# Optimization experiments

Measured on AMD Instinct MI355X. Metric: run time of the kernel, lower is better.

The kernel has to match this reference:

```python
import math
import jax, jax.numpy as jnp
import numpy as np

B, T, C, H = 2, 2048, 1024, 16
D = C // H


def get_slopes(n):
    def pow2_slopes(n):
        start = 2.0 ** (-(2.0 ** (-(math.log2(n) - 3))))
        return [start * (start ** i) for i in range(n)]
    if math.log2(n).is_integer():
        return pow2_slopes(n)
    c = 2 ** math.floor(math.log2(n))
    return pow2_slopes(c) + get_slopes(2 * c)[0::2][: n - c]


def setup_inputs() -> dict:
    key = jax.random.key(0)
    ks = jax.random.split(key, 5)
    std = 0.02
    x = jax.random.normal(ks[0], (B, T, C), dtype=jnp.float32)
    Wq = std * jax.random.normal(ks[1], (C, C), dtype=jnp.float32)
    Wk = std * jax.random.normal(ks[2], (C, C), dtype=jnp.float32)
    Wv = std * jax.random.normal(ks[3], (C, C), dtype=jnp.float32)
    Wo = (std / math.sqrt(24)) * jax.random.normal(ks[4], (C, C), dtype=jnp.float32)
    z = jnp.zeros((C,), dtype=jnp.float32)
    return {"x": x, "Wq": Wq, "bq": z, "Wk": Wk, "bk": z, "Wv": Wv, "bv": z, "Wo": Wo, "bo": z}


def reference(x, Wq, bq, Wk, bk, Wv, bv, Wo, bo):
    b, t, c = x.shape
    h, d = H, c // H
    # qkv projections: nn.Linear computes x @ W.T + b
    q = (x @ Wq.T + bq).reshape(b, t, h, d).transpose(0, 2, 1, 3)  # [B,H,T,D]
    k = (x @ Wk.T + bk).reshape(b, t, h, d).transpose(0, 2, 1, 3)
    v = (x @ Wv.T + bv).reshape(b, t, h, d).transpose(0, 2, 1, 3)

    att = jnp.einsum("bhqd,bhkd->bhqk", q, k) * (1.0 / math.sqrt(d))

    # ALiBi bias: -slope_h * (i - j) on the lower triangle, 0 above
    slopes = jnp.asarray(get_slopes(h), dtype=x.dtype)  # [H]
    i = jnp.arange(t)
    rel = jnp.tril(i[:, None] - i[None, :]).astype(x.dtype)  # [T,T]
    alibi = -slopes[:, None, None] * rel  # [H,T,T]
    att = att + alibi[None, :, :, :]

    causal = jnp.tril(jnp.ones((t, t), dtype=bool))
    att = jnp.where(causal[None, None, :, :], att, -jnp.inf)
    att = jax.nn.softmax(att, axis=-1)

    y = jnp.einsum("bhqk,bhkd->bhqd", att, v)
    y = y.transpose(0, 2, 1, 3).reshape(b, t, c)
    return y @ Wo.T + bo
```

## Files before the change

### kernel.cpp

```cpp
#include <hip/hip_runtime.h>
#include <hip/hip_bf16.h>
#include <cstdint>
#include <cstddef>

#define B_ 2
#define T_ 2048
#define C_ 1024
#define H_ 16
#define D_ 64
#define BT_ (B_*T_)
#define QKV_S 3072

typedef __bf16 bf16;
typedef __bf16 bf16x4 __attribute__((ext_vector_type(4)));
typedef __bf16 bf16x8 __attribute__((ext_vector_type(8)));
typedef float f32x4 __attribute__((ext_vector_type(4)));

__global__ __launch_bounds__(256) void cast_f32_bf16(const float* __restrict__ in,
                                                     bf16* __restrict__ out, int n) {
  int stride = gridDim.x * blockDim.x;
  for (int i = blockIdx.x * blockDim.x + threadIdx.x; i * 4 < n; i += stride) {
    float4 v = *reinterpret_cast<const float4*>(in + (size_t)i * 4);
    bf16x4 o;
    o[0] = (bf16)v.x; o[1] = (bf16)v.y; o[2] = (bf16)v.z; o[3] = (bf16)v.w;
    *reinterpret_cast<bf16x4*>(out + (size_t)i * 4) = o;
  }
}

template<typename OutT>
__global__ __launch_bounds__(256) void gemm_bt(const bf16* __restrict__ A,
                                               const bf16* __restrict__ Bm,
                                               const float* __restrict__ bias,
                                               OutT* __restrict__ Cout,
                                               int M, int N, int K) {
  __shared__ bf16 As[128 * 32];
  __shared__ bf16 Bs[128 * 32];
  const int tid = threadIdx.x;
  const int wid = tid >> 6, lane = tid & 63;
  const int grp = lane >> 4, li = lane & 15;
  const int wr = wid >> 1, wc = wid & 1;
  const int m0 = blockIdx.y * 128, n0 = blockIdx.x * 128;

  f32x4 acc[4][4] = {};

  const int srow = lane >> 2;
  const int scol = (lane & 3) * 8;

  for (int k0 = 0; k0 < K; k0 += 32) {
#pragma unroll
    for (int p = 0; p < 2; ++p) {
      const int rbase = (p * 4 + wid) * 16;
      const bf16* ga = A + (size_t)(m0 + rbase + srow) * K + (k0 + scol);
      const bf16* gb = Bm + (size_t)(n0 + rbase + srow) * K + (k0 + scol);
      bf16* la = As + (p * 4 + wid) * 512;
      bf16* lb = Bs + (p * 4 + wid) * 512;
      __builtin_amdgcn_global_load_lds((__attribute__((address_space(1))) void*)ga,
                                       (__attribute__((address_space(3))) void*)la, 16, 0, 0);
      __builtin_amdgcn_global_load_lds((__attribute__((address_space(1))) void*)gb,
                                       (__attribute__((address_space(3))) void*)lb, 16, 0, 0);
    }
    __syncthreads();

    bf16x8 af[4], bfr[4];
#pragma unroll
    for (int m = 0; m < 4; ++m)
      af[m] = *reinterpret_cast<const bf16x8*>(&As[(wr * 64 + m * 16 + li) * 32 + grp * 8]);
#pragma unroll
    for (int n = 0; n < 4; ++n)
      bfr[n] = *reinterpret_cast<const bf16x8*>(&Bs[(wc * 64 + n * 16 + li) * 32 + grp * 8]);
#pragma unroll
    for (int m = 0; m < 4; ++m)
#pragma unroll
      for (int n = 0; n < 4; ++n)
        acc[m][n] = __builtin_amdgcn_mfma_f32_16x16x32_bf16(af[m], bfr[n], acc[m][n], 0, 0, 0);
    __syncthreads();
  }

  float bcol[4];
#pragma unroll
  for (int n = 0; n < 4; ++n) bcol[n] = bias[n0 + wc * 64 + n * 16 + li];
#pragma unroll
  for (int m = 0; m < 4; ++m) {
#pragma unroll
    for (int n = 0; n < 4; ++n) {
      const int col = n0 + wc * 64 + n * 16 + li;
#pragma unroll
      for (int j = 0; j < 4; ++j) {
        const int row = m0 + wr * 64 + m * 16 + grp * 4 + j;
        float v = acc[m][n][j] + bcol[n];
        Cout[(size_t)row * N + col] = (OutT)v;
      }
    }
  }
}

__global__ __launch_bounds__(256) void transpose_v(const bf16* __restrict__ qkv,
                                                   bf16* __restrict__ Vt) {
  __shared__ bf16 tile[64 * 72];
  const int tid = threadIdx.x;
  const int t0 = blockIdx.x * 64, bh = blockIdx.y;
  const int b = bh >> 4, h = bh & 15;
#pragma unroll
  for (int p = 0; p < 2; ++p) {
    int idx = p * 256 + tid;
    int r = idx >> 3, c = (idx & 7) * 8;
    bf16x8 v = *reinterpret_cast<const bf16x8*>(qkv + (size_t)(b * T_ + t0 + r) * QKV_S + 2 * C_ + h * D_ + c);
    *reinterpret_cast<bf16x8*>(&tile[r * 72 + c]) = v;
  }
  __syncthreads();
#pragma unroll
  for (int p = 0; p < 2; ++p) {
    int idx = p * 256 + tid;
    int d = idx >> 3, tc = (idx & 7) * 8;
    bf16x8 o;
#pragma unroll
    for (int j = 0; j < 8; ++j) o[j] = tile[(tc + j) * 72 + d];
    *reinterpret_cast<bf16x8*>(Vt + ((size_t)bh * D_ + d) * T_ + t0 + tc) = o;
  }
}

__global__ __launch_bounds__(512) void attn_kernel(const bf16* __restrict__ qkv,
                                                   const bf16* __restrict__ Vt,
                                                   bf16* __restrict__ Y) {
  __shared__ bf16 Ks[2][64 * 64];
  __shared__ bf16 Vs[2][64 * 64];
  __shared__ bf16 Ps[8 * 16 * 72];

  const int tid = threadIdx.x;
  const int wid = tid >> 6, lane = tid & 63;
  const int grp = lane >> 4, li = lane & 15;
  const int QT = gridDim.x - 1 - blockIdx.x;
  const int bh = blockIdx.y;
  const int b = bh >> 4, h = bh & 15;
  const int q0 = QT * 128;
  const int wq0 = q0 + wid * 16;
  const int qi = wq0 + li;
  const float slope = exp2f(-0.5f * (float)(h + 1));

  bf16* Pw = Ps + wid * (16 * 72);

  bf16x8 qf[2];
  {
    const bf16* qrow = qkv + (size_t)(b * T_ + qi) * QKV_S + h * D_;
    qf[0] = *reinterpret_cast<const bf16x8*>(qrow + grp * 8);
    qf[1] = *reinterpret_cast<const bf16x8*>(qrow + 32 + grp * 8);
#pragma unroll
    for (int c = 0; c < 2; ++c)
#pragma unroll
      for (int j = 0; j < 8; ++j)
        qf[c][j] = (bf16)((float)qf[c][j] * 0.125f);
  }

  f32x4 oacc[4] = {};
  float mrun = -1e30f, lrun = 0.f;

  const bf16* Kbase = qkv + (size_t)b * T_ * QKV_S + C_ + (size_t)h * D_;
  const bf16* Vbase = Vt + (size_t)bh * D_ * T_;

  const int strow = tid >> 3;
  const int stswz = ((tid & 7) * 16) ^ ((strow & 7) << 4);
  const int rsw = (li & 7) << 4;

  auto stage = [&](int kv0, int bufi) __attribute__((always_inline)) {
    const bf16* gk = Kbase + (size_t)(kv0 + strow) * QKV_S + (stswz >> 1);
    const bf16* gv = Vbase + (size_t)strow * T_ + kv0 + (stswz >> 1);
    __builtin_amdgcn_global_load_lds((__attribute__((address_space(1))) void*)gk,
                                     (__attribute__((address_space(3))) void*)(&Ks[bufi][wid * 512]), 16, 0, 0);
    __builtin_amdgcn_global_load_lds((__attribute__((address_space(1))) void*)gv,
                                     (__attribute__((address_space(3))) void*)(&Vs[bufi][wid * 512]), 16, 0, 0);
  };

  auto compute = [&](int kv0, int bufi, bool masked) __attribute__((always_inline)) {
    const char* Kb = (const char*)&Ks[bufi][0];
    const char* Vb = (const char*)&Vs[bufi][0];

    f32x4 s[4] = {};
    __builtin_amdgcn_s_setprio(1);
#pragma unroll
    for (int n = 0; n < 4; ++n) {
      const char* kr = Kb + (n * 16 + li) * 128;
      bf16x8 kf0 = *reinterpret_cast<const bf16x8*>(kr + ((grp * 16) ^ rsw));
      bf16x8 kf1 = *reinterpret_cast<const bf16x8*>(kr + ((64 + grp * 16) ^ rsw));
      s[n] = __builtin_amdgcn_mfma_f32_16x16x32_bf16(kf0, qf[0], s[n], 0, 0, 0);
      s[n] = __builtin_amdgcn_mfma_f32_16x16x32_bf16(kf1, qf[1], s[n], 0, 0, 0);
    }
    __builtin_amdgcn_s_setprio(0);

    float p[4][4];
    float rm = -1e30f;
#pragma unroll
    for (int n = 0; n < 4; ++n)
#pragma unroll
      for (int j = 0; j < 4; ++j) {
        const int kv = kv0 + n * 16 + grp * 4 + j;
        float sv = fmaf(-slope, (float)(qi - kv), s[n][j]);
        if (masked) sv = (kv <= qi) ? sv : -1e30f;
        p[n][j] = sv;
        rm = fmaxf(rm, sv);
      }
    rm = fmaxf(rm, __shfl_xor(rm, 16, 64));
    rm = fmaxf(rm, __shfl_xor(rm, 32, 64));
    const float mnew = fmaxf(mrun, rm);
    const float alpha = __expf(mrun - mnew);
    mrun = mnew;
    float rs = 0.f;
#pragma unroll
    for (int n = 0; n < 4; ++n)
#pragma unroll
      for (int j = 0; j < 4; ++j) {
        float e = __expf(p[n][j] - mnew);
        p[n][j] = e;
        rs += e;
      }
    rs += __shfl_xor(rs, 16, 64);
    rs += __shfl_xor(rs, 32, 64);
    lrun = lrun * alpha + rs;
#pragma unroll
    for (int nd = 0; nd < 4; ++nd)
#pragma unroll
      for (int j = 0; j < 4; ++j)
        oacc[nd][j] *= alpha;

#pragma unroll
    for (int n = 0; n < 4; ++n) {
      bf16x4 p4;
#pragma unroll
      for (int j = 0; j < 4; ++j) p4[j] = (bf16)p[n][j];
      *reinterpret_cast<bf16x4*>(Pw + li * 72 + n * 16 + grp * 4) = p4;
    }
    asm volatile("s_waitcnt lgkmcnt(0)" ::: "memory");
    __builtin_amdgcn_sched_barrier(0);

    __builtin_amdgcn_s_setprio(1);
#pragma unroll
    for (int kc = 0; kc < 2; ++kc) {
      bf16x8 pb = *reinterpret_cast<const bf16x8*>(Pw + li * 72 + kc * 32 + grp * 8);
#pragma unroll
      for (int nd = 0; nd < 4; ++nd) {
        const char* vrp = Vb + (nd * 16 + li) * 128;
        bf16x8 vf = *reinterpret_cast<const bf16x8*>(vrp + ((kc * 64 + grp * 16) ^ rsw));
        oacc[nd] = __builtin_amdgcn_mfma_f32_16x16x32_bf16(vf, pb, oacc[nd], 0, 0, 0);
      }
    }
    __builtin_amdgcn_s_setprio(0);
  };

  const int nt = 2 * QT + 2;
  stage(0, 0);
  __syncthreads();
  int cur = 0;
  for (int t = 0; t < nt; ++t) {
    const int kv0 = t * 64;
    if (t + 1 < nt) stage((t + 1) * 64, cur ^ 1);
    if (kv0 <= wq0) compute(kv0, cur, kv0 + 64 > wq0);
    __syncthreads();
    cur ^= 1;
  }

  const float rinv = 1.f / lrun;
#pragma unroll
  for (int nd = 0; nd < 4; ++nd) {
    bf16x4 o4;
#pragma unroll
    for (int j = 0; j < 4; ++j) o4[j] = (bf16)(oacc[nd][j] * rinv);
    *reinterpret_cast<bf16x4*>(Pw + li * 72 + nd * 16 + grp * 4) = o4;
  }
  asm volatile("s_waitcnt lgkmcnt(0)" ::: "memory");
  __builtin_amdgcn_sched_barrier(0);
  {
    bf16* yrow = Y + (size_t)(b * T_ + qi) * C_ + h * D_;
#pragma unroll
    for (int c = 0; c < 2; ++c) {
      bf16x8 y8 = *reinterpret_cast<const bf16x8*>(Pw + li * 72 + (c * 4 + grp) * 8);
      *reinterpret_cast<bf16x8*>(yrow + (c * 4 + grp) * 8) = y8;
    }
  }
}

extern "C" void kernel_launch(void* const* d_in, const int* in_sizes, int n_in,
                              void* d_out, int out_size, void* d_ws, size_t ws_size,
                              hipStream_t stream) {
  const float* x  = (const float*)d_in[0];
  const float* Wq = (const float*)d_in[1];
  const float* bq = (const float*)d_in[2];
  const float* Wk = (const float*)d_in[3];
  const float* bk = (const float*)d_in[4];
  const float* Wv = (const float*)d_in[5];
  const float* bv = (const float*)d_in[6];
  const float* Wo = (const float*)d_in[7];
  const float* bo = (const float*)d_in[8];
  float* out = (float*)d_out;

  char* ws = (char*)d_ws;
  bf16* xb    = (bf16*)ws; ws += (size_t)BT_ * C_ * 2;
  bf16* wqkvb = (bf16*)ws; ws += (size_t)3 * C_ * C_ * 2;
  bf16* wob   = (bf16*)ws; ws += (size_t)C_ * C_ * 2;
  bf16* qkvb  = (bf16*)ws; ws += (size_t)BT_ * QKV_S * 2;
  bf16* vtb   = (bf16*)ws; ws += (size_t)B_ * H_ * D_ * T_ * 2;
  float* bqkv = (float*)ws; ws += (size_t)3 * C_ * 4;
  bf16* yb    = xb;

  hipMemcpyAsync(bqkv,          bq, C_ * 4, hipMemcpyDeviceToDevice, stream);
  hipMemcpyAsync(bqkv + C_,     bk, C_ * 4, hipMemcpyDeviceToDevice, stream);
  hipMemcpyAsync(bqkv + 2 * C_, bv, C_ * 4, hipMemcpyDeviceToDevice, stream);

  auto cast = [&](const float* src, bf16* dst, int n) {
    int thr = n / 4;
    int blocks = (thr + 255) / 256;
    if (blocks > 4096) blocks = 4096;
    cast_f32_bf16<<<dim3(blocks), dim3(256), 0, stream>>>(src, dst, n);
  };
  cast(x,  xb,  BT_ * C_);
  cast(Wq, wqkvb,               C_ * C_);
  cast(Wk, wqkvb + C_ * C_,     C_ * C_);
  cast(Wv, wqkvb + 2 * C_ * C_, C_ * C_);
  cast(Wo, wob, C_ * C_);

  gemm_bt<bf16><<<dim3(QKV_S / 128, BT_ / 128), dim3(256), 0, stream>>>(xb, wqkvb, bqkv, qkvb, BT_, QKV_S, C_);

  transpose_v<<<dim3(T_ / 64, B_ * H_), dim3(256), 0, stream>>>(qkvb, vtb);

  attn_kernel<<<dim3(T_ / 128, B_ * H_), dim3(512), 0, stream>>>(qkvb, vtb, yb);

  gemm_bt<float><<<dim3(C_ / 128, BT_ / 128), dim3(256), 0, stream>>>(yb, wob, bo, out, BT_, C_, C_);
}
```

Baseline: 243.2 us.

## Fuse casts, double-buffer GEMM, fuse V transpose into QKV GEMM, use exp2 softmax

Merges the five cast launches into one kernel and double-buffers the GEMM's LDS tiles so the next K-slice loads while MFMAs run. The QKV GEMM epilogue writes V directly in transposed layout, which removes the separate transpose kernel and its round trip through memory. The attention softmax moves to the exp2 domain with a precomputed ALiBi offset table to save per-element ALU work. The costs are double the GEMM's LDS, more registers for the offset table, and scattered 8-byte stores in the V epilogue.

Result: no change. 238.6 us (-1.9%).

```diff
diff --git a/kernel.cpp b/kernel.cpp
--- a/kernel.cpp
+++ b/kernel.cpp
@@ -10,31 +10,52 @@
 #define D_ 64
 #define BT_ (B_*T_)
 #define QKV_S 3072
+#define LOG2E 1.4426950408889634f
 
 typedef __bf16 bf16;
 typedef __bf16 bf16x4 __attribute__((ext_vector_type(4)));
 typedef __bf16 bf16x8 __attribute__((ext_vector_type(8)));
 typedef float f32x4 __attribute__((ext_vector_type(4)));
 
-__global__ __launch_bounds__(256) void cast_f32_bf16(const float* __restrict__ in,
-                                                     bf16* __restrict__ out, int n) {
-  int stride = gridDim.x * blockDim.x;
-  for (int i = blockIdx.x * blockDim.x + threadIdx.x; i * 4 < n; i += stride) {
-    float4 v = *reinterpret_cast<const float4*>(in + (size_t)i * 4);
-    bf16x4 o;
-    o[0] = (bf16)v.x; o[1] = (bf16)v.y; o[2] = (bf16)v.z; o[3] = (bf16)v.w;
-    *reinterpret_cast<bf16x4*>(out + (size_t)i * 4) = o;
-  }
+__global__ __launch_bounds__(256) void cast_all(const float* __restrict__ x,
+                                                const float* __restrict__ wq,
+                                                const float* __restrict__ wk,
+                                                const float* __restrict__ wv,
+                                                const float* __restrict__ wo,
+                                                bf16* __restrict__ xb,
+                                                bf16* __restrict__ wqkvb,
+                                                bf16* __restrict__ wob) {
+  const int X4 = (BT_ * C_) / 4;
+  const int W4 = (C_ * C_) / 4;
+  int i = blockIdx.x * blockDim.x + threadIdx.x;
+  if (i >= X4 + 4 * W4) return;
+  const float* src;
+  bf16* dst;
+  int off;
+  if (i < X4) {
+    src = x; dst = xb; off = i;
+  } else {
+    int k = i - X4;
+    int w = k >> 18;
+    off = k & (W4 - 1);
+    src = (w == 0) ? wq : (w == 1) ? wk : (w == 2) ? wv : wo;
+    dst = (w < 3) ? (wqkvb + (size_t)w * C_ * C_) : wob;
+  }
+  float4 v = reinterpret_cast<const float4*>(src)[off];
+  bf16x4 o;
+  o[0] = (bf16)v.x; o[1] = (bf16)v.y; o[2] = (bf16)v.z; o[3] = (bf16)v.w;
+  *reinterpret_cast<bf16x4*>(dst + (size_t)off * 4) = o;
 }
 
-template<typename OutT>
+template<typename OutT, bool FUSE_VT>
 __global__ __launch_bounds__(256) void gemm_bt(const bf16* __restrict__ A,
                                                const bf16* __restrict__ Bm,
                                                const float* __restrict__ bias,
                                                OutT* __restrict__ Cout,
+                                               bf16* __restrict__ VtOut,
                                                int M, int N, int K) {
-  __shared__ bf16 As[128 * 32];
-  __shared__ bf16 Bs[128 * 32];
+  __shared__ bf16 As[2][128 * 32];
+  __shared__ bf16 Bs[2][128 * 32];
   const int tid = threadIdx.x;
   const int wid = tid >> 6, lane = tid & 63;
   const int grp = lane >> 4, li = lane & 15;
@@ -46,76 +67,75 @@
   const int srow = lane >> 2;
   const int scol = (lane & 3) * 8;
 
-  for (int k0 = 0; k0 < K; k0 += 32) {
+  auto stage = [&](int k0, int bufi) __attribute__((always_inline)) {
 #pragma unroll
     for (int p = 0; p < 2; ++p) {
       const int rbase = (p * 4 + wid) * 16;
       const bf16* ga = A + (size_t)(m0 + rbase + srow) * K + (k0 + scol);
       const bf16* gb = Bm + (size_t)(n0 + rbase + srow) * K + (k0 + scol);
-      bf16* la = As + (p * 4 + wid) * 512;
-      bf16* lb = Bs + (p * 4 + wid) * 512;
       __builtin_amdgcn_global_load_lds((__attribute__((address_space(1))) void*)ga,
-                                       (__attribute__((address_space(3))) void*)la, 16, 0, 0);
+                                       (__attribute__((address_space(3))) void*)(&As[bufi][(p * 4 + wid) * 512]), 16, 0, 0);
       __builtin_amdgcn_global_load_lds((__attribute__((address_space(1))) void*)gb,
-                                       (__attribute__((address_space(3))) void*)lb, 16, 0, 0);
-    }
-    __syncthreads();
+                                       (__attribute__((address_space(3))) void*)(&Bs[bufi][(p * 4 + wid) * 512]), 16, 0, 0);
+    }
+  };
+
+  const int nt = K >> 5;
+  stage(0, 0);
+  __syncthreads();
+  int cur = 0;
+  for (int t = 0; t < nt; ++t) {
+    if (t + 1 < nt) stage((t + 1) * 32, cur ^ 1);
 
     bf16x8 af[4], bfr[4];
 #pragma unroll
     for (int m = 0; m < 4; ++m)
-      af[m] = *reinterpret_cast<const bf16x8*>(&As[(wr * 64 + m * 16 + li) * 32 + grp * 8]);
+      af[m] = *reinterpret_cast<const bf16x8*>(&As[cur][(wr * 64 + m * 16 + li) * 32 + grp * 8]);
 #pragma unroll
     for (int n = 0; n < 4; ++n)
-      bfr[n] = *reinterpret_cast<const bf16x8*>(&Bs[(wc * 64 + n * 16 + li) * 32 + grp * 8]);
+      bfr[n] = *reinterpret_cast<const bf16x8*>(&Bs[cur][(wc * 64 + n * 16 + li) * 32 + grp * 8]);
 #pragma unroll
     for (int m = 0; m < 4; ++m)
 #pragma unroll
       for (int n = 0; n < 4; ++n)
         acc[m][n] = __builtin_amdgcn_mfma_f32_16x16x32_bf16(af[m], bfr[n], acc[m][n], 0, 0, 0);
+
     __syncthreads();
+    cur ^= 1;
   }
 
   float bcol[4];
 #pragma unroll
   for (int n = 0; n < 4; ++n) bcol[n] = bias[n0 + wc * 64 + n * 16 + li];
-#pragma unroll
-  for (int m = 0; m < 4; ++m) {
-#pragma unroll
-    for (int n = 0; n < 4; ++n) {
-      const int col = n0 + wc * 64 + n * 16 + li;
-#pragma unroll
-      for (int j = 0; j < 4; ++j) {
-        const int row = m0 + wr * 64 + m * 16 + grp * 4 + j;
-        float v = acc[m][n][j] + bcol[n];
-        Cout[(size_t)row * N + col] = (OutT)v;
-      }
-    }
-  }
-}
-
-__global__ __launch_bounds__(256) void transpose_v(const bf16* __restrict__ qkv,
-                                                   bf16* __restrict__ Vt) {
-  __shared__ bf16 tile[64 * 72];
-  const int tid = threadIdx.x;
-  const int t0 = blockIdx.x * 64, bh = blockIdx.y;
-  const int b = bh >> 4, h = bh & 15;
-#pragma unroll
-  for (int p = 0; p < 2; ++p) {
-    int idx = p * 256 + tid;
-    int r = idx >> 3, c = (idx & 7) * 8;
-    bf16x8 v = *reinterpret_cast<const bf16x8*>(qkv + (size_t)(b * T_ + t0 + r) * QKV_S + 2 * C_ + h * D_ + c);
-    *reinterpret_cast<bf16x8*>(&tile[r * 72 + c]) = v;
-  }
-  __syncthreads();
-#pragma unroll
-  for (int p = 0; p < 2; ++p) {
-    int idx = p * 256 + tid;
-    int d = idx >> 3, tc = (idx & 7) * 8;
-    bf16x8 o;
-#pragma unroll
-    for (int j = 0; j < 8; ++j) o[j] = tile[(tc + j) * 72 + d];
-    *reinterpret_cast<bf16x8*>(Vt + ((size_t)bh * D_ + d) * T_ + t0 + tc) = o;
+
+  if (FUSE_VT && n0 >= 2 * C_) {
+#pragma unroll
+    for (int m = 0; m < 4; ++m) {
+      const int row0 = m0 + wr * 64 + m * 16 + grp * 4;
+      const int b = row0 >> 11, t = row0 & (T_ - 1);
+#pragma unroll
+      for (int n = 0; n < 4; ++n) {
+        const int hd = (n0 - 2 * C_) + wc * 64 + n * 16 + li;
+        bf16x4 o4;
+#pragma unroll
+        for (int j = 0; j < 4; ++j) o4[j] = (bf16)(acc[m][n][j] + bcol[n]);
+        *reinterpret_cast<bf16x4*>(VtOut + ((size_t)(b * C_ + hd)) * T_ + t) = o4;
+      }
+    }
+  } else {
+#pragma unroll
+    for (int m = 0; m < 4; ++m) {
+#pragma unroll
+      for (int n = 0; n < 4; ++n) {
+        const int col = n0 + wc * 64 + n * 16 + li;
+#pragma unroll
+        for (int j = 0; j < 4; ++j) {
+          const int row = m0 + wr * 64 + m * 16 + grp * 4 + j;
+          float v = acc[m][n][j] + bcol[n];
+          Cout[(size_t)row * N + col] = (OutT)v;
+        }
+      }
+    }
   }
 }
 
@@ -135,7 +155,7 @@
   const int q0 = QT * 128;
   const int wq0 = q0 + wid * 16;
   const int qi = wq0 + li;
-  const float slope = exp2f(-0.5f * (float)(h + 1));
+  const float slope2 = exp2f(-0.5f * (float)(h + 1)) * LOG2E;
 
   bf16* Pw = Ps + wid * (16 * 72);
 
@@ -150,6 +170,14 @@
       for (int j = 0; j < 8; ++j)
         qf[c][j] = (bf16)((float)qf[c][j] * 0.125f);
   }
+
+  float off[4][4];
+#pragma unroll
+  for (int n = 0; n < 4; ++n)
+#pragma unroll
+    for (int j = 0; j < 4; ++j)
+      off[n][j] = slope2 * (float)(n * 16 + grp * 4 + j);
+  const float bb = -slope2 * (float)qi;
 
   f32x4 oacc[4] = {};
   float mrun = -1e30f, lrun = 0.f;
@@ -186,29 +214,32 @@
     }
     __builtin_amdgcn_s_setprio(0);
 
+    const float base = fmaf(slope2, (float)kv0, bb);
     float p[4][4];
     float rm = -1e30f;
 #pragma unroll
     for (int n = 0; n < 4; ++n)
 #pragma unroll
       for (int j = 0; j < 4; ++j) {
-        const int kv = kv0 + n * 16 + grp * 4 + j;
-        float sv = fmaf(-slope, (float)(qi - kv), s[n][j]);
-        if (masked) sv = (kv <= qi) ? sv : -1e30f;
+        float sv = fmaf(s[n][j], LOG2E, base + off[n][j]);
+        if (masked) {
+          const int kv = kv0 + n * 16 + grp * 4 + j;
+          sv = (kv <= qi) ? sv : -1e30f;
+        }
         p[n][j] = sv;
         rm = fmaxf(rm, sv);
       }
     rm = fmaxf(rm, __shfl_xor(rm, 16, 64));
     rm = fmaxf(rm, __shfl_xor(rm, 32, 64));
     const float mnew = fmaxf(mrun, rm);
-    const float alpha = __expf(mrun - mnew);
+    const float alpha = exp2f(mrun - mnew);
     mrun = mnew;
     float rs = 0.f;
 #pragma unroll
     for (int n = 0; n < 4; ++n)
 #pragma unroll
       for (int j = 0; j < 4; ++j) {
-        float e = __expf(p[n][j] - mnew);
+        float e = exp2f(p[n][j] - mnew);
         p[n][j] = e;
         rs += e;
       }
@@ -304,23 +335,16 @@
   hipMemcpyAsync(bqkv + C_,     bk, C_ * 4, hipMemcpyDeviceToDevice, stream);
   hipMemcpyAsync(bqkv + 2 * C_, bv, C_ * 4, hipMemcpyDeviceToDevice, stream);
 
-  auto cast = [&](const float* src, bf16* dst, int n) {
-    int thr = n / 4;
-    int blocks = (thr + 255) / 256;
-    if (blocks > 4096) blocks = 4096;
-    cast_f32_bf16<<<dim3(blocks), dim3(256), 0, stream>>>(src, dst, n);
-  };
-  cast(x,  xb,  BT_ * C_);
-  cast(Wq, wqkvb,               C_ * C_);
-  cast(Wk, wqkvb + C_ * C_,     C_ * C_);
-  cast(Wv, wqkvb + 2 * C_ * C_, C_ * C_);
-  cast(Wo, wob, C_ * C_);
-
-  gemm_bt<bf16><<<dim3(QKV_S / 128, BT_ / 128), dim3(256), 0, stream>>>(xb, wqkvb, bqkv, qkvb, BT_, QKV_S, C_);
-
-  transpose_v<<<dim3(T_ / 64, B_ * H_), dim3(256), 0, stream>>>(qkvb, vtb);
+  {
+    const int total4 = (BT_ * C_ + 4 * C_ * C_) / 4;
+    cast_all<<<dim3(total4 / 256), dim3(256), 0, stream>>>(x, Wq, Wk, Wv, Wo, xb, wqkvb, wob);
+  }
+
+  gemm_bt<bf16, true><<<dim3(QKV_S / 128, BT_ / 128), dim3(256), 0, stream>>>(
+      xb, wqkvb, bqkv, qkvb, vtb, BT_, QKV_S, C_);
 
   attn_kernel<<<dim3(T_ / 128, B_ * H_), dim3(512), 0, stream>>>(qkvb, vtb, yb);
 
-  gemm_bt<float><<<dim3(C_ / 128, BT_ / 128), dim3(256), 0, stream>>>(yb, wob, bo, out, BT_, C_, C_);
+  gemm_bt<float, false><<<dim3(C_ / 128, BT_ / 128), dim3(256), 0, stream>>>(
+      yb, wob, bo, out, nullptr, BT_, C_, C_);
 }
```
